# Optimization experiments

Hardware: AMD Instinct MI355X
Metric: run time of the kernel (lower is better)

Reference implementation:

```python
import jax, jax.numpy as jnp
import numpy as np

BS, N, C = 512, 18, 2048
EPS = 1e-12
BN_SCALE = 1.0 / np.sqrt(1.0 + 1e-5)  # eval-mode BN with running_mean=0, running_var=1


def _normalize(v):
    # F.normalize(p=2, dim=2, eps=1e-12)
    n = jnp.linalg.norm(v, axis=2, keepdims=True)
    return v / jnp.maximum(n, EPS)


def _bn_relu(v, gamma, beta):
    # BatchNorm2d in eval mode (running_mean=0, running_var=1) followed by ReLU
    return jax.nn.relu(v * (gamma * BN_SCALE) + beta)


def _safe_sqrt(r):
    # forward-identical to sqrt (r >= 0 here); avoids NaN grad at r == 0 (diagonal)
    pos = r > 0
    return jnp.where(pos, jnp.sqrt(jnp.where(pos, r, 1.0)), 0.0)


def setup_inputs() -> dict:
    key = jax.random.key(0)
    ks = jax.random.split(key, 10)
    s = 0.02
    return {
        "x": jax.random.normal(ks[0], (BS, N, C), jnp.float32),
        "part_coordinate": jax.random.uniform(ks[1], (BS, N, 4), jnp.float32),
        # conv1: C -> 3 (1x1)
        "w1": jax.random.normal(ks[2], (3, C), jnp.float32) * s,
        "b1": jnp.zeros((3,), jnp.float32),
        # conv2: 4 -> C, BN, ReLU, C -> 3
        "w2a": jax.random.normal(ks[3], (C, 4), jnp.float32) * s,
        "b2a": jnp.zeros((C,), jnp.float32),
        "g2": jnp.ones((C,), jnp.float32),
        "be2": jnp.zeros((C,), jnp.float32),
        "w2b": jax.random.normal(ks[4], (3, C), jnp.float32) * s,
        "b2b": jnp.zeros((3,), jnp.float32),
        # conv: C -> C, BN, ReLU
        "wc": jax.random.normal(ks[5], (C, C), jnp.float32) * s,
        "bc": jnp.zeros((C,), jnp.float32),
        "gc": jnp.ones((C,), jnp.float32),
        "bec": jnp.zeros((C,), jnp.float32),
        # conv3: C -> C, BN, ReLU
        "w3": jax.random.normal(ks[6], (C, C), jnp.float32) * s,
        "b3": jnp.zeros((C,), jnp.float32),
        "g3": jnp.ones((C,), jnp.float32),
        "be3": jnp.zeros((C,), jnp.float32),
    }


def reference(x, part_coordinate, w1, b1, w2a, b2a, g2, be2, w2b, b2b,
              wc, bc, gc, bec, w3, b3, g3, be3):
    # z1 = softmax(conv1(x)) over the 3 clusters
    z1 = jax.nn.softmax(jnp.einsum('bnc,kc->bnk', x, w1) + b1, axis=2)  # [B,N,3]

    # distance_list1: cosine affinities of x and z1
    xn = _normalize(x)
    d1_1 = jnp.einsum('bnc,bmc->bnm', xn, xn)       # [B,N,N]
    z1n = _normalize(z1)
    d2_1 = jnp.einsum('bnk,bmk->bnm', z1n, z1n)     # [B,N,N]

    # z2 = softmax(conv2(part_coordinate))
    h = _bn_relu(jnp.einsum('bnf,cf->bnc', part_coordinate, w2a) + b2a, g2, be2)
    z2 = jax.nn.softmax(jnp.einsum('bnc,kc->bnk', h, w2b) + b2b, axis=2)  # [B,N,3]

    # distance_list2: spatial-center distance + cosine affinity of z2
    yc = part_coordinate[..., 0] + jnp.floor(part_coordinate[..., 2] / 2)
    xc = part_coordinate[..., 1] + jnp.floor(part_coordinate[..., 3] / 2)
    dy = (yc[:, None, :] - yc[:, :, None]) ** 2
    dx = (xc[:, None, :] - xc[:, :, None]) ** 2
    d1_2 = 1.0 - 2.0 * _safe_sqrt(dx + dy)          # [B,N,N]
    z2n = _normalize(z2)
    d2_2 = jnp.einsum('bnk,bmk->bnm', z2n, z2n)     # [B,N,N]

    # encode / decode aggregation over 3 cluster nodes
    z = z1 + z2                                      # [B,N,3]
    enc = z / (jnp.sum(z, axis=1, keepdims=True) + EPS)
    dec = z / (jnp.sum(z, axis=2, keepdims=True) + EPS)
    u = jnp.einsum('bnk,bnc->bkc', enc, x)           # [B,3,C]
    u = _bn_relu(jnp.einsum('bkc,dc->bkd', u, wc) + bc, gc, bec)
    y = jnp.einsum('bnk,bkc->bnc', dec, u)           # [B,N,C]
    y = _bn_relu(jnp.einsum('bnc,dc->bnd', y, w3) + b3, g3, be3) + x

    return (y, d2_1, d1_1, d2_2, d1_2)
```

## Files before the change

kernel.cpp:

```cpp
#include <hip/hip_runtime.h>

#define BS   512
#define NPTS 18
#define CH   2048
#define EPSF 1e-12f
#define BNS  0.9999950000374997f

typedef unsigned short ushort_t;
typedef __attribute__((ext_vector_type(8)))  short bfrag;
typedef __attribute__((ext_vector_type(4)))  float f32x4v;
typedef __attribute__((ext_vector_type(16))) float f32x16;

__device__ inline ushort_t bf16_rne(float f) {
  union { float f; unsigned int u; } c; c.f = f;
  unsigned int u = c.u;
  u += 0x7fffu + ((u >> 16) & 1u);
  return (ushort_t)(u >> 16);
}
__device__ inline float bf16_to_f(ushort_t s) {
  union { float f; unsigned int u; } c; c.u = ((unsigned int)s) << 16;
  return c.f;
}
__device__ inline bfrag cvt8(float4 a, float4 b) {
  bfrag r;
  r[0]=(short)bf16_rne(a.x); r[1]=(short)bf16_rne(a.y);
  r[2]=(short)bf16_rne(a.z); r[3]=(short)bf16_rne(a.w);
  r[4]=(short)bf16_rne(b.x); r[5]=(short)bf16_rne(b.y);
  r[6]=(short)bf16_rne(b.z); r[7]=(short)bf16_rne(b.w);
  return r;
}

__global__ __launch_bounds__(1024, 4) void k_mega(
    const float* __restrict__ x, const float* __restrict__ pc,
    const float* __restrict__ w1, const float* __restrict__ b1,
    const float* __restrict__ w2a, const float* __restrict__ b2a,
    const float* __restrict__ g2, const float* __restrict__ be2,
    const float* __restrict__ w2b, const float* __restrict__ b2b,
    const float* __restrict__ wc, const float* __restrict__ w3,
    ushort_t* __restrict__ wc_bf, ushort_t* __restrict__ w3_bf,
    float* __restrict__ d21, float* __restrict__ d11,
    float* __restrict__ d22, float* __restrict__ d12,
    ushort_t* __restrict__ u_pre, float* __restrict__ dec_out)
{
  const int blk = blockIdx.x, tid = threadIdx.x;

  if (blk >= BS) {
    const int cb = blk - BS;
    const int n4 = CH*CH/4;
    #pragma unroll
    for (int k = 0; k < 4; k++) {
      int gid = cb*4096 + k*1024 + tid;
      const float* src; ushort_t* dst; int i;
      if (gid < n4) { src = wc; dst = wc_bf; i = gid; }
      else          { src = w3; dst = w3_bf; i = gid - n4; }
      float4 v = ((const float4*)src)[i];
      ushort4 o;
      o.x = bf16_rne(v.x); o.y = bf16_rne(v.y);
      o.z = bf16_rne(v.z); o.w = bf16_rne(v.w);
      ((ushort4*)dst)[i] = o;
    }
    return;
  }

  __shared__ __align__(16) ushort_t IMG[21*CH];
  __shared__ float Gt[4][378];
  __shared__ float l2part[9][18];
  __shared__ float sGl[378], l2s[54];
  __shared__ float z1s[54], z2s[54], encs[54];
  __shared__ float ycs[NPTS], xcs[NPTS];
  __shared__ float n1inv[NPTS], n2inv[NPTS], rinvS[NPTS], colinv[3];

  const int b = blk, lane = tid & 63, wv = tid >> 6;

  {
    const float4* x4 = (const float4*)x + (size_t)b*9216;
    #pragma unroll
    for (int k = 0; k < 4; k++) {
      int p = k*1024 + tid;
      float4 a = x4[2*p], c = x4[2*p + 1];
      int row = p >> 8;
      *(bfrag*)((char*)IMG + ((p*16) ^ ((row & 7) << 4))) = cvt8(a, c);
    }
    if (tid < 512) {
      int p = 4096 + tid;
      float4 a = x4[2*p], c = x4[2*p + 1];
      int row = p >> 8;
      *(bfrag*)((char*)IMG + ((p*16) ^ ((row & 7) << 4))) = cvt8(a, c);
    }
    if (tid < 768) {
      int p = tid;
      const float4* w4 = (const float4*)w1;
      float4 a = w4[2*p], c = w4[2*p + 1];
      int row = 18 + (p >> 8);
      *(bfrag*)((char*)IMG + ((73728 + p*16) ^ ((row & 7) << 4))) = cvt8(a, c);
    }
  }
  __syncthreads();

  if (wv < 4) {
    const int rc = lane & 31, kh = lane >> 5;
    const int arow = (rc < NPTS) ? rc : (NPTS-1);
    const int brow = (rc < 21) ? rc : 20;
    const int amsk = (arow & 7) << 4, bmsk = (brow & 7) << 4;
    const int abase = arow*4096, bbase = brow*4096;
    f32x16 acc0 = {0.f,0.f,0.f,0.f,0.f,0.f,0.f,0.f,0.f,0.f,0.f,0.f,0.f,0.f,0.f,0.f};
    f32x16 acc1 = acc0;
    #pragma unroll 4
    for (int j = 0; j < 32; j++) {
      const int kb = (wv*512 + j*16 + kh*8)*2;
      bfrag av = *(const bfrag*)((const char*)IMG + ((abase + kb) ^ amsk));
      bfrag bv = *(const bfrag*)((const char*)IMG + ((bbase + kb) ^ bmsk));
      if (j & 1) acc1 = __builtin_amdgcn_mfma_f32_32x32x16_bf16(av, bv, acc1, 0, 0, 0);
      else       acc0 = __builtin_amdgcn_mfma_f32_32x32x16_bf16(av, bv, acc0, 0, 0, 0);
    }
    #pragma unroll
    for (int r = 0; r < 16; r++) {
      int orow = (r & 3) + 8*(r >> 2) + 4*kh;
      if (orow < NPTS && rc < 21) Gt[wv][orow*21 + rc] = acc0[r] + acc1[r];
    }
  } else if (wv < 13) {
    const int zid = wv - 4, g = zid/3, th = zid - 3*g;
    const int cs = (th == 0) ? 0 : (th == 1) ? 683 : 1366;
    const int ce = (th == 0) ? 683 : (th == 1) ? 1366 : 2048;
    const float* pcb = pc + (size_t)b*NPTS*4 + g*24;
    float pq[6][4];
    #pragma unroll
    for (int j = 0; j < 6; j++) {
      pq[j][0] = pcb[j*4+0]; pq[j][1] = pcb[j*4+1];
      pq[j][2] = pcb[j*4+2]; pq[j][3] = pcb[j*4+3];
    }
    float acc[6][3];
    #pragma unroll
    for (int j = 0; j < 6; j++) { acc[j][0]=0.f; acc[j][1]=0.f; acc[j][2]=0.f; }
    for (int c = cs + lane; c < ce; c += 64) {
      const float4 wa = *(const float4*)(w2a + (size_t)c*4);
      float bb = b2a[c], gg = g2[c]*BNS, be = be2[c];
      float wb0 = w2b[c], wb1 = w2b[CH+c], wb2 = w2b[2*CH+c];
      #pragma unroll
      for (int j = 0; j < 6; j++) {
        float v = fmaf(pq[j][3], wa.w, fmaf(pq[j][2], wa.z,
                  fmaf(pq[j][1], wa.y, fmaf(pq[j][0], wa.x, bb))));
        float h = fmaxf(fmaf(v, gg, be), 0.f);
        acc[j][0] = fmaf(h, wb0, acc[j][0]);
        acc[j][1] = fmaf(h, wb1, acc[j][1]);
        acc[j][2] = fmaf(h, wb2, acc[j][2]);
      }
    }
    #pragma unroll
    for (int j = 0; j < 6; j++)
      #pragma unroll
      for (int k = 0; k < 3; k++) {
        float v = acc[j][k];
        #pragma unroll
        for (int off = 32; off; off >>= 1) v += __shfl_xor(v, off);
        if (lane == 0) l2part[zid][j*3 + k] = v;
      }
  }
  __syncthreads();

  if (tid < 378) {
    sGl[tid] = (Gt[0][tid] + Gt[1][tid]) + (Gt[2][tid] + Gt[3][tid]);
  } else if (tid < 432) {
    int t = tid - 378;
    int p = t/3, k = t - 3*p, g = p/6, pp = p - 6*g;
    l2s[t] = l2part[g*3][pp*3+k] + l2part[g*3+1][pp*3+k] + l2part[g*3+2][pp*3+k]
             + b2b[k];
  } else if (tid >= 448 && tid < 466) {
    int n = tid - 448;
    const float* p = pc + (size_t)b*NPTS*4 + n*4;
    ycs[n] = p[0] + floorf(p[2]*0.5f);
    xcs[n] = p[1] + floorf(p[3]*0.5f);
  }
  __syncthreads();

  if (tid < NPTS) {
    int n = tid;
    float a0 = sGl[n*21+18] + b1[0], a1 = sGl[n*21+19] + b1[1], a2 = sGl[n*21+20] + b1[2];
    float mx = fmaxf(a0, fmaxf(a1, a2));
    float e0 = expf(a0-mx), e1 = expf(a1-mx), e2 = expf(a2-mx);
    float inv = 1.f/(e0+e1+e2);
    float z10 = e0*inv, z11 = e1*inv, z12 = e2*inv;
    z1s[n*3+0]=z10; z1s[n*3+1]=z11; z1s[n*3+2]=z12;
    n1inv[n] = 1.f/fmaxf(sqrtf(z10*z10+z11*z11+z12*z12), EPSF);

    float c0 = l2s[n*3+0], c1 = l2s[n*3+1], c2 = l2s[n*3+2];
    mx = fmaxf(c0, fmaxf(c1, c2));
    e0 = expf(c0-mx); e1 = expf(c1-mx); e2 = expf(c2-mx);
    inv = 1.f/(e0+e1+e2);
    float z20 = e0*inv, z21 = e1*inv, z22 = e2*inv;
    z2s[n*3+0]=z20; z2s[n*3+1]=z21; z2s[n*3+2]=z22;
    n2inv[n] = 1.f/fmaxf(sqrtf(z20*z20+z21*z21+z22*z22), EPSF);

    float zr0 = z10+z20, zr1 = z11+z21, zr2 = z12+z22;
    float rinvv = 1.f/((zr0+zr1+zr2) + EPSF);
    dec_out[(size_t)b*54 + n*3 + 0] = zr0*rinvv;
    dec_out[(size_t)b*54 + n*3 + 1] = zr1*rinvv;
    dec_out[(size_t)b*54 + n*3 + 2] = zr2*rinvv;

    rinvS[n] = 1.f/fmaxf(sqrtf(sGl[n*21+n]), EPSF);
  }
  __syncthreads();

  if (tid < 3) {
    float s = 0.f;
    #pragma unroll
    for (int n = 0; n < NPTS; n++) s += z1s[n*3+tid] + z2s[n*3+tid];
    colinv[tid] = 1.f/(s + EPSF);
  }
  if (tid < NPTS*NPTS) {
    int t = tid;
    int n = t/NPTS, mm = t - n*NPTS;
    float dd21 = (z1s[n*3]*z1s[mm*3] + z1s[n*3+1]*z1s[mm*3+1] + z1s[n*3+2]*z1s[mm*3+2])
                 * n1inv[n]*n1inv[mm];
    float dd22 = (z2s[n*3]*z2s[mm*3] + z2s[n*3+1]*z2s[mm*3+1] + z2s[n*3+2]*z2s[mm*3+2])
                 * n2inv[n]*n2inv[mm];
    float dd11 = sGl[n*21+mm] * rinvS[n]*rinvS[mm];
    float dyv = ycs[mm]-ycs[n], dxv = xcs[mm]-xcs[n];
    float r = dxv*dxv + dyv*dyv;
    float dd12 = 1.f - 2.f*((r > 0.f) ? sqrtf(r) : 0.f);
    size_t o = (size_t)b*NPTS*NPTS + t;
    d21[o] = dd21; d11[o] = dd11; d22[o] = dd22; d12[o] = dd12;
  }
  __syncthreads();
  if (tid < 54) encs[tid] = (z1s[tid]+z2s[tid])*colinv[tid%3];
  __syncthreads();

  {
    const int c0 = tid*2;
    float a0=0.f,a1=0.f,a2=0.f, q0=0.f,q1=0.f,q2=0.f;
    #pragma unroll
    for (int n = 0; n < NPTS; n++) {
      unsigned v = *(const unsigned*)((const char*)IMG + ((n*4096 + c0*2) ^ ((n & 7) << 4)));
      float x0 = bf16_to_f((ushort_t)(v & 0xffff));
      float x1 = bf16_to_f((ushort_t)(v >> 16));
      float e0 = encs[n*3+0], e1 = encs[n*3+1], e2 = encs[n*3+2];
      a0 = fmaf(e0, x0, a0); q0 = fmaf(e0, x1, q0);
      a1 = fmaf(e1, x0, a1); q1 = fmaf(e1, x1, q1);
      a2 = fmaf(e2, x0, a2); q2 = fmaf(e2, x1, q2);
    }
    ushort2 o0, o1, o2;
    o0.x = bf16_rne(a0); o0.y = bf16_rne(q0);
    o1.x = bf16_rne(a1); o1.y = bf16_rne(q1);
    o2.x = bf16_rne(a2); o2.y = bf16_rne(q2);
    *(ushort2*)(u_pre + ((size_t)b*3 + 0)*CH + c0) = o0;
    *(ushort2*)(u_pre + ((size_t)b*3 + 1)*CH + c0) = o1;
    *(ushort2*)(u_pre + ((size_t)b*3 + 2)*CH + c0) = o2;
  }
}

#define GM 1536
#define GK 2048
#define GN 2048

#define STAGE(buf, k0) { \
    _Pragma("unroll") \
    for (int i = 0; i < 4; i++) \
      __builtin_amdgcn_global_load_lds( \
          (const __attribute__((address_space(1))) void*)(Ag + (size_t)(i*32 + ldrow)*GK + (k0)), \
          (__attribute__((address_space(3))) void*)(&Asm[buf][i*2048 + wv*512]), 16, 0, 0); \
    _Pragma("unroll") \
    for (int i = 0; i < 2; i++) \
      __builtin_amdgcn_global_load_lds( \
          (const __attribute__((address_space(1))) void*)(Bg + (size_t)(i*32 + ldrow)*GK + (k0)), \
          (__attribute__((address_space(3))) void*)(&Bsm[buf][i*2048 + wv*512]), 16, 0, 0); }

template<int MODE>
__global__ __launch_bounds__(256) void gemm_mfma(
    const ushort_t* __restrict__ A, const ushort_t* __restrict__ B,
    void* __restrict__ Cout, const float* __restrict__ bias,
    const float* __restrict__ gamma, const float* __restrict__ beta)
{
  __shared__ ushort_t Asm[2][128*64];
  __shared__ ushort_t Bsm[2][64*64];
  const int tid  = threadIdx.x;
  const int lane = tid & 63, wv = tid >> 6;
  const int mb = blockIdx.x % (GM/128), nb = blockIdx.x / (GM/128);
  const int wr = (wv >> 1) * 64, wc = (wv & 1) * 32;

  f32x4v acc[4][2];
  #pragma unroll
  for (int m = 0; m < 4; m++)
    #pragma unroll
    for (int n = 0; n < 2; n++)
      acc[m][n] = (f32x4v){0.f, 0.f, 0.f, 0.f};

  const int ldrow = tid >> 3;
  const int ldcol = (((tid & 7) ^ (ldrow & 7)) * 8);
  const ushort_t* Ag = A + (size_t)(mb*128)*GK + ldcol;
  const ushort_t* Bg = B + (size_t)(nb*64)*GK + ldcol;
  const int r15 = lane & 15, khi = lane >> 4;

  STAGE(0, 0)
  __syncthreads();
  for (int t = 0; t < GK/64; ++t) {
    const int cur = t & 1;
    if (t < GK/64 - 1) STAGE(cur ^ 1, (t+1)*64)
    #pragma unroll
    for (int ks = 0; ks < 2; ks++) {
      bfrag af[4], bfv[2];
      #pragma unroll
      for (int m = 0; m < 4; m++) {
        const int ar = wr + m*16 + r15;
        af[m] = *(const bfrag*)(&Asm[cur][ar*64 + ((ks*32 + khi*8) ^ ((ar & 7)*8))]);
      }
      #pragma unroll
      for (int n = 0; n < 2; n++) {
        const int br = wc + n*16 + r15;
        bfv[n] = *(const bfrag*)(&Bsm[cur][br*64 + ((ks*32 + khi*8) ^ ((br & 7)*8))]);
      }
      #pragma unroll
      for (int m = 0; m < 4; m++)
        #pragma unroll
        for (int n = 0; n < 2; n++)
          acc[m][n] = __builtin_amdgcn_mfma_f32_16x16x32_bf16(
              af[m], bfv[n], acc[m][n], 0, 0, 0);
    }
    __syncthreads();
  }

  #pragma unroll
  for (int n = 0; n < 2; n++) {
    const int gc = nb*64 + wc + n*16 + r15;
    float bi = 0.f, ga = 0.f, be = 0.f;
    if (MODE == 1) { bi = bias[gc]; ga = gamma[gc]*BNS; be = beta[gc]; }
    #pragma unroll
    for (int m = 0; m < 4; m++) {
      const int gr0 = mb*128 + wr + m*16 + khi*4;
      #pragma unroll
      for (int r = 0; r < 4; r++) {
        float v = acc[m][n][r];
        if (MODE == 1) {
          v = fmaxf(fmaf(v + bi, ga, be), 0.f);
          ((ushort_t*)Cout)[(size_t)(gr0 + r)*GN + gc] = bf16_rne(v);
        } else {
          ((float*)Cout)[(size_t)(gr0 + r)*GN + gc] = v;
        }
      }
    }
  }
}

__global__ __launch_bounds__(256) void k_epi(
    const float* __restrict__ x, const float* __restrict__ V,
    const float* __restrict__ dec, const float* __restrict__ b3,
    const float* __restrict__ g3, const float* __restrict__ be3,
    float* __restrict__ y)
{
  __shared__ float4 lv[3*512];
  __shared__ float4 lmul[512], ladd[512];
  __shared__ float ld[54];
  const int b = blockIdx.x, tid = threadIdx.x;

  const float4* v4 = (const float4*)(V + (size_t)b*3*CH);
  for (int i = tid; i < 1536; i += 256) lv[i] = v4[i];
  const float4* g34  = (const float4*)g3;
  const float4* b34  = (const float4*)b3;
  const float4* be34 = (const float4*)be3;
  for (int i = tid; i < 512; i += 256) {
    float4 g = g34[i], bb = b34[i], be = be34[i];
    float4 mu, ad;
    mu.x = g.x*BNS; mu.y = g.y*BNS; mu.z = g.z*BNS; mu.w = g.w*BNS;
    ad.x = fmaf(bb.x, mu.x, be.x); ad.y = fmaf(bb.y, mu.y, be.y);
    ad.z = fmaf(bb.z, mu.z, be.z); ad.w = fmaf(bb.w, mu.w, be.w);
    lmul[i] = mu; ladd[i] = ad;
  }
  if (tid < 54) ld[tid] = dec[(size_t)b*54 + tid];
  __syncthreads();

  for (int r = 0; r < NPTS; r++) {
    float d0 = ld[r*3+0], d1 = ld[r*3+1], d2 = ld[r*3+2];
    const float4* xr = (const float4*)(x + ((size_t)b*NPTS + r)*CH);
    float4* yr = (float4*)(y + ((size_t)b*NPTS + r)*CH);
    for (int i = tid; i < 512; i += 256) {
      float4 v0 = lv[i], v1 = lv[512+i], v2 = lv[1024+i];
      float4 mu = lmul[i], ad = ladd[i], xa = xr[i];
      float4 o;
      o.x = fmaxf(fmaf(fmaf(d0,v0.x, fmaf(d1,v1.x, d2*v2.x)), mu.x, ad.x), 0.f) + xa.x;
      o.y = fmaxf(fmaf(fmaf(d0,v0.y, fmaf(d1,v1.y, d2*v2.y)), mu.y, ad.y), 0.f) + xa.y;
      o.z = fmaxf(fmaf(fmaf(d0,v0.z, fmaf(d1,v1.z, d2*v2.z)), mu.z, ad.z), 0.f) + xa.z;
      o.w = fmaxf(fmaf(fmaf(d0,v0.w, fmaf(d1,v1.w, d2*v2.w)), mu.w, ad.w), 0.f) + xa.w;
      yr[i] = o;
    }
  }
}

extern "C" void kernel_launch(void* const* d_in, const int* in_sizes, int n_in,
                              void* d_out, int out_size, void* d_ws, size_t ws_size,
                              hipStream_t stream) {
  const float* x   = (const float*)d_in[0];
  const float* pc  = (const float*)d_in[1];
  const float* w1  = (const float*)d_in[2];
  const float* b1  = (const float*)d_in[3];
  const float* w2a = (const float*)d_in[4];
  const float* b2a = (const float*)d_in[5];
  const float* g2  = (const float*)d_in[6];
  const float* be2 = (const float*)d_in[7];
  const float* w2b = (const float*)d_in[8];
  const float* b2b = (const float*)d_in[9];
  const float* wc  = (const float*)d_in[10];
  const float* bc  = (const float*)d_in[11];
  const float* gc  = (const float*)d_in[12];
  const float* bec = (const float*)d_in[13];
  const float* w3  = (const float*)d_in[14];
  const float* b3  = (const float*)d_in[15];
  const float* g3  = (const float*)d_in[16];
  const float* be3 = (const float*)d_in[17];

  float* out = (float*)d_out;
  float* y   = out;
  float* d21 = out + (size_t)BS*NPTS*CH;
  float* d11 = d21 + (size_t)BS*NPTS*NPTS;
  float* d22 = d11 + (size_t)BS*NPTS*NPTS;
  float* d12 = d22 + (size_t)BS*NPTS*NPTS;

  char* ybytes = (char*)y;
  ushort_t* u_pre_bf = (ushort_t*)(ybytes + 0);
  ushort_t* u_bf     = (ushort_t*)(ybytes + 6291456);
  ushort_t* wc_bf    = (ushort_t*)(ybytes + 12582912);
  ushort_t* w3_bf    = (ushort_t*)(ybytes + 20971520);

  float* V    = (float*)d_ws;
  float* decb = V + (size_t)BS*3*CH;

  k_mega<<<BS + 512, 1024, 0, stream>>>(x, pc, w1, b1, w2a, b2a, g2, be2,
                                        w2b, b2b, wc, w3, wc_bf, w3_bf,
                                        d21, d11, d22, d12, u_pre_bf, decb);
  gemm_mfma<1><<<(GM/128)*(GN/64), 256, 0, stream>>>(u_pre_bf, wc_bf, u_bf, bc, gc, bec);
  gemm_mfma<0><<<(GM/128)*(GN/64), 256, 0, stream>>>(u_bf, w3_bf, V, nullptr, nullptr, nullptr);
  k_epi<<<BS, 256, 0, stream>>>(x, V, decb, b3, g3, be3, y);
}
```

Baseline: 150.8 us.

## Shrink shared memory footprint and raise launch-bound occupancy to eight blocks

Removes the w1 rows from the shared bf16 image: lanes that handle the conv1 columns now load w1 straight from global memory and convert it inside the MFMA loop. All small float scratch arrays are packed into a single 2048-float buffer, and the partial Gram sums are reduced in place. The launch bound's minimum blocks per SM goes from 4 to 8. Together these cut LDS usage per block so more blocks can be resident. The cost is per-iteration global loads and bf16 conversion in three lanes, which makes those waves diverge, plus tighter register limits that could cause spills.

```diff
diff --git a/kernel.cpp b/kernel.cpp
--- a/kernel.cpp
+++ b/kernel.cpp
@@ -30,7 +30,7 @@
   return r;
 }
 
-__global__ __launch_bounds__(1024, 4) void k_mega(
+__global__ __launch_bounds__(1024, 8) void k_mega(
     const float* __restrict__ x, const float* __restrict__ pc,
     const float* __restrict__ w1, const float* __restrict__ b1,
     const float* __restrict__ w2a, const float* __restrict__ b2a,
@@ -62,13 +62,20 @@
     return;
   }
 
-  __shared__ __align__(16) ushort_t IMG[21*CH];
-  __shared__ float Gt[4][378];
-  __shared__ float l2part[9][18];
-  __shared__ float sGl[378], l2s[54];
-  __shared__ float z1s[54], z2s[54], encs[54];
-  __shared__ float ycs[NPTS], xcs[NPTS];
-  __shared__ float n1inv[NPTS], n2inv[NPTS], rinvS[NPTS], colinv[3];
+  __shared__ __align__(16) ushort_t IMG[18*CH];
+  __shared__ __align__(16) float F[2048];
+  float* Gt     = F;
+  float* l2part = F + 1512;
+  float* l2s    = F + 1674;
+  float* z1s    = F + 1728;
+  float* z2s    = F + 1782;
+  float* encs   = F + 1836;
+  float* ycs    = F + 1890;
+  float* xcs    = F + 1908;
+  float* n1inv  = F + 1926;
+  float* n2inv  = F + 1944;
+  float* rinvS  = F + 1962;
+  float* colinv = F + 1980;
 
   const int b = blk, lane = tid & 63, wv = tid >> 6;
 
@@ -87,36 +94,32 @@
       int row = p >> 8;
       *(bfrag*)((char*)IMG + ((p*16) ^ ((row & 7) << 4))) = cvt8(a, c);
     }
-    if (tid < 768) {
-      int p = tid;
-      const float4* w4 = (const float4*)w1;
-      float4 a = w4[2*p], c = w4[2*p + 1];
-      int row = 18 + (p >> 8);
-      *(bfrag*)((char*)IMG + ((73728 + p*16) ^ ((row & 7) << 4))) = cvt8(a, c);
-    }
   }
   __syncthreads();
 
   if (wv < 4) {
     const int rc = lane & 31, kh = lane >> 5;
     const int arow = (rc < NPTS) ? rc : (NPTS-1);
-    const int brow = (rc < 21) ? rc : 20;
-    const int amsk = (arow & 7) << 4, bmsk = (brow & 7) << 4;
-    const int abase = arow*4096, bbase = brow*4096;
+    const int amsk = (arow & 7) << 4;
+    const int abase = arow*4096;
+    const bool isw = (rc >= NPTS) && (rc < NPTS+3);
+    const int wrow = isw ? (rc - NPTS) : 0;
+    const float* wp = w1 + (size_t)wrow*CH + wv*512 + kh*8;
     f32x16 acc0 = {0.f,0.f,0.f,0.f,0.f,0.f,0.f,0.f,0.f,0.f,0.f,0.f,0.f,0.f,0.f,0.f};
     f32x16 acc1 = acc0;
     #pragma unroll 4
     for (int j = 0; j < 32; j++) {
       const int kb = (wv*512 + j*16 + kh*8)*2;
       bfrag av = *(const bfrag*)((const char*)IMG + ((abase + kb) ^ amsk));
-      bfrag bv = *(const bfrag*)((const char*)IMG + ((bbase + kb) ^ bmsk));
+      bfrag bv = av;
+      if (isw) bv = cvt8(*(const float4*)(wp + j*16), *(const float4*)(wp + j*16 + 4));
       if (j & 1) acc1 = __builtin_amdgcn_mfma_f32_32x32x16_bf16(av, bv, acc1, 0, 0, 0);
       else       acc0 = __builtin_amdgcn_mfma_f32_32x32x16_bf16(av, bv, acc0, 0, 0, 0);
     }
     #pragma unroll
     for (int r = 0; r < 16; r++) {
       int orow = (r & 3) + 8*(r >> 2) + 4*kh;
-      if (orow < NPTS && rc < 21) Gt[wv][orow*21 + rc] = acc0[r] + acc1[r];
+      if (orow < NPTS && rc < 21) Gt[wv*378 + orow*21 + rc] = acc0[r] + acc1[r];
     }
   } else if (wv < 13) {
     const int zid = wv - 4, g = zid/3, th = zid - 3*g;
@@ -153,18 +156,18 @@
         float v = acc[j][k];
         #pragma unroll
         for (int off = 32; off; off >>= 1) v += __shfl_xor(v, off);
-        if (lane == 0) l2part[zid][j*3 + k] = v;
+        if (lane == 0) l2part[zid*18 + j*3 + k] = v;
       }
   }
   __syncthreads();
 
   if (tid < 378) {
-    sGl[tid] = (Gt[0][tid] + Gt[1][tid]) + (Gt[2][tid] + Gt[3][tid]);
+    F[tid] = (F[tid] + F[378+tid]) + (F[756+tid] + F[1134+tid]);
   } else if (tid < 432) {
     int t = tid - 378;
     int p = t/3, k = t - 3*p, g = p/6, pp = p - 6*g;
-    l2s[t] = l2part[g*3][pp*3+k] + l2part[g*3+1][pp*3+k] + l2part[g*3+2][pp*3+k]
-             + b2b[k];
+    l2s[t] = l2part[(g*3)*18 + pp*3+k] + l2part[(g*3+1)*18 + pp*3+k]
+           + l2part[(g*3+2)*18 + pp*3+k] + b2b[k];
   } else if (tid >= 448 && tid < 466) {
     int n = tid - 448;
     const float* p = pc + (size_t)b*NPTS*4 + n*4;
@@ -172,6 +175,7 @@
     xcs[n] = p[1] + floorf(p[3]*0.5f);
   }
   __syncthreads();
+  float* sGl = F;
 
   if (tid < NPTS) {
     int n = tid;
```

Result: faster. 146.5 us (-2.9%).
